# Performance work log

Hardware: AMD Instinct MI355X
Metric: run time of the kernel (lower is better)

The kernel has to match this reference:

```python
import jax, jax.numpy as jnp
import numpy as np

WEIGHT = 1.0
EPS = 1e-10


def _high_mask(h, w):
    # Boolean mask: True = high-frequency region (outside center rectangle after fftshift)
    mask = np.ones((h, w), dtype=np.float32)
    ch, cw = h // 2, w // 2
    mask[ch - h // 8: ch + h // 8, cw - w // 8: cw + w // 8] = 0.0
    return jnp.asarray(mask)


def _high_freq_psd(img):
    # img: (B, 3, H, W) in [-1, 1] -> per-image mean log10 PSD over high-freq region, shape (B,)
    gray = 0.299 * img[:, 0] + 0.587 * img[:, 1] + 0.114 * img[:, 2]  # (B, H, W)
    gray = (gray + 1.0) / 2.0
    fft = jnp.fft.fft2(gray)                       # batched complex FFT over last two dims
    fft = jnp.fft.fftshift(fft, axes=(-2, -1))
    psd_log = jnp.log10(jnp.abs(fft) ** 2 + EPS)   # (B, H, W)
    h, w = gray.shape[-2:]
    mask = _high_mask(h, w)
    return jnp.sum(psd_log * mask, axis=(-2, -1)) / jnp.sum(mask)


def setup_inputs() -> dict:
    key = jax.random.key(0)
    k1, k2 = jax.random.split(key)
    B, C, H, W = 32, 3, 512, 512
    generated = jax.random.normal(k1, (B, C, H, W), dtype=jnp.float32)
    target = jax.random.normal(k2, (B, C, H, W), dtype=jnp.float32)
    return {"generated": generated, "target": target}


def reference(generated, target):
    psd_gen = _high_freq_psd(generated)      # (B,)
    psd_target = _high_freq_psd(target)      # (B,)
    loss = jnp.mean(jnp.abs(psd_gen - psd_target))  # F.l1_loss
    return WEIGHT * loss
```

## Files before the change

### kernel.cpp

```cpp
#include <hip/hip_runtime.h>
#include <hip/hip_bf16.h>
#include <hip/hip_fp16.h>
#include <math.h>


__device__ double g_partials[64 * 33 * 4];
__device__ __align__(16) __half2 g_wsfall[256 * 512];

__device__ __forceinline__ float2 cadd(float2 a, float2 b){ return make_float2(a.x+b.x, a.y+b.y); }
__device__ __forceinline__ float2 csub(float2 a, float2 b){ return make_float2(a.x-b.x, a.y-b.y); }
__device__ __forceinline__ float2 cmul(float2 a, float2 b){
  return make_float2(fmaf(a.x, b.x, -(a.y*b.y)), fmaf(a.x, b.y, a.y*b.x));
}
__device__ __forceinline__ float2 mul_mi(float2 a){ return make_float2(a.y, -a.x); }

__device__ __forceinline__ void fft8(float2 v[8]){
  const float S = 0.70710678118654752440f;
  float2 c0=cadd(v[0],v[4]), c1=cadd(v[1],v[5]), c2=cadd(v[2],v[6]), c3=cadd(v[3],v[7]);
  float2 d0=csub(v[0],v[4]);
  float2 t1=csub(v[1],v[5]);
  float2 d1=make_float2(S*(t1.x+t1.y), S*(t1.y-t1.x));
  float2 d2=mul_mi(csub(v[2],v[6]));
  float2 t3=csub(v[3],v[7]);
  float2 d3=make_float2(S*(t3.y-t3.x), -S*(t3.x+t3.y));
  float2 e0=cadd(c0,c2), e1=cadd(c1,c3), f0=csub(c0,c2), f1=mul_mi(csub(c1,c3));
  float2 g0=cadd(d0,d2), g1=cadd(d1,d3), h0=csub(d0,d2), h1=mul_mi(csub(d1,d3));
  v[0]=cadd(e0,e1); v[4]=csub(e0,e1);
  v[2]=cadd(f0,f1); v[6]=csub(f0,f1);
  v[1]=cadd(g0,g1); v[5]=csub(g0,g1);
  v[3]=cadd(h0,h1); v[7]=csub(h0,h1);
}

__device__ __forceinline__ void twiddle8(float2 v[8], float ang){
  float sn, cs;
  __sincosf(ang, &sn, &cs);
  float2 w = make_float2(cs, sn);
  float2 wp = w;
  v[1] = cmul(v[1], wp);
  #pragma unroll
  for (int m = 2; m < 8; ++m){ wp = cmul(wp, w); v[m] = cmul(v[m], wp); }
}

__device__ __forceinline__ int padi(int i){ return i + (i >> 3); }

__device__ __forceinline__ void lds_fence(){
  asm volatile("s_waitcnt lgkmcnt(0)" ::: "memory");
  __builtin_amdgcn_sched_barrier(0);
}

__device__ __forceinline__ void fft512(float2 v[8], float* re, float* im, int t){
  const float TW = -6.28318530717958647692f;
  fft8(v);
  twiddle8(v, TW * (float)t * (1.0f/512.0f));
  lds_fence();
  #pragma unroll
  for (int m = 0; m < 8; ++m){ int a = padi(m*64 + t); re[a] = v[m].x; im[a] = v[m].y; }
  lds_fence();
  const int q = t >> 3, n = t & 7;
  #pragma unroll
  for (int j = 0; j < 8; ++j){ int a = padi(q*64 + n + 8*j); v[j].x = re[a]; v[j].y = im[a]; }
  fft8(v);
  twiddle8(v, TW * (float)n * (1.0f/64.0f));
  lds_fence();
  #pragma unroll
  for (int m = 0; m < 8; ++m){ int a = padi(q*64 + m*8 + n); re[a] = v[m].x; im[a] = v[m].y; }
  lds_fence();
  #pragma unroll
  for (int j = 0; j < 8; ++j){ int a = padi(q*64 + n*8 + j); v[j].x = re[a]; v[j].y = im[a]; }
  fft8(v);
}

#define GRAY1(r,g,b) ((fmaf(0.299f,(r), fmaf(0.587f,(g), 0.114f*(b))) + 1.0f)*0.5f)

__device__ __forceinline__ void dma_pair(const float* base, float* st, int t){
  #pragma unroll
  for (int ch = 0; ch < 3; ++ch){
    const float* pb = base + ch * 262144 + 4*t;
    float* lb = st + ch*1024;
    #pragma unroll
    for (int seg = 0; seg < 4; ++seg){
      __builtin_amdgcn_global_load_lds(
        (const __attribute__((address_space(1))) void*)(pb + seg*256),
        (__attribute__((address_space(3))) void*)(lb + seg*256),
        16, 0, 0);
    }
  }
}

__global__ __launch_bounds__(128)
void k_rowfft(const float* __restrict__ gen, const float* __restrict__ tgt,
              __half2* ws, int img0){
  __half2* w = ws ? ws : g_wsfall;
  const int wg   = blockIdx.x;
  const int imgl = wg >> 4;
  const int bl   = wg & 15;
  const int img  = img0 + imgl;
  const int wave = threadIdx.x >> 6, t = threadIdx.x & 63;
  const int prB  = bl*16 + wave*8;
  const float* src = (img < 32) ? gen : tgt;
  const float* base0 = src + (size_t)(img & 31) * 786432 + (size_t)prB * 1024;

  __shared__ float stage_all[2][2][3072];
  float* stg0 = stage_all[wave][0];
  float* stg1 = stage_all[wave][1];

  const int off = 8*(t & 7) + (t >> 3);

  dma_pair(base0, stg0, t);
  #pragma unroll
  for (int n = 0; n < 8; ++n){
    float* stc = (n & 1) ? stg1 : stg0;
    float* stn = (n & 1) ? stg0 : stg1;
    lds_fence();
    if (n < 7) dma_pair(base0 + (size_t)(n+1)*1024, stn, t);
    if (n == 0)      { asm volatile("s_waitcnt vmcnt(12)" ::: "memory"); }
    else if (n < 7)  { asm volatile("s_waitcnt vmcnt(20)" ::: "memory"); }
    else             { asm volatile("s_waitcnt vmcnt(8)"  ::: "memory"); }
    __builtin_amdgcn_sched_barrier(0);

    float2 v[8];
    #pragma unroll
    for (int j = 0; j < 8; ++j){
      const int x = t + 64*j;
      v[j] = make_float2(GRAY1(stc[x],     stc[1024+x], stc[2048+x]),
                         GRAY1(stc[512+x], stc[1536+x], stc[2560+x]));
    }
    fft512(v, stc, stc + 1024, t);

    __half2* dst = w + ((size_t)imgl * 256 + (prB + n)) * 512;
    #pragma unroll
    for (int j = 0; j < 8; ++j) dst[64*j + off] = __floats2half2_rn(v[j].x, v[j].y);
  }
}

__global__ __launch_bounds__(256)
void k_colfft(const __half2* __restrict__ ws, int img0){
  const __half2* w = ws ? ws : (const __half2*)g_wsfall;
  const int wg   = blockIdx.x;
  const int imgl = wg / 33;
  const int blk  = wg - imgl * 33;
  const int img  = img0 + imgl;
  const int kx0  = blk * 8;
  const int tid  = threadIdx.x;
  const int wave = tid >> 6, t = tid & 63;
  const int ncols = (blk == 32) ? 1 : 8;

  __shared__ float2 own[8][260], mir[8][260];
  __shared__ float re_all[4][576], im_all[4][576];
  float* re = re_all[wave];
  float* im = im_all[wave];

  const __half2* zb = w + (size_t)imgl * 131072;
  #pragma unroll
  for (int it = 0; it < 8; ++it){
    const int idx = it*256 + tid;
    const int p = idx >> 3, e = idx & 7;
    own[e][p] = __half22float2(zb[p*512 + kx0 + e]);
    mir[e][p] = __half22float2(zb[p*512 + ((512 - (kx0 + e)) & 511)]);
  }
  __syncthreads();

  double acc = 0.0;
  for (int ci = 0; ci < 2; ++ci){
    const int e = wave*2 + ci;
    if (e < ncols){
      const int kx = kx0 + e;
      const bool sub_own = (kx <= 63);
      const bool sub_mir = (kx >= 1) & (kx <= 64);
      const float base = (kx == 0 || kx == 256) ? 1.0f : 2.0f;

      float2 v[8];
      const int u = t >> 1;
      const bool odd = (t & 1);
      #pragma unroll
      for (int j = 0; j < 8; ++j){
        const int p = u + 32*j;
        float2 A = own[e][p];
        float2 B = mir[e][p]; B.y = -B.y;
        float2 Fe = make_float2((A.x + B.x)*0.5f, (A.y + B.y)*0.5f);
        float2 Fo = mul_mi(make_float2((A.x - B.x)*0.5f, (A.y - B.y)*0.5f));
        v[j] = odd ? Fo : Fe;
      }
      fft512(v, re, im, t);

      #pragma unroll
      for (int j = 0; j < 8; ++j){
        const bool inS  = (j == 0) | (j == 7);
        const bool inSp = (j == 0) | ((j == 1) & (t == 0)) | ((j == 7) & (t != 0));
        float wgt = base;
        if (sub_own & inS)  wgt -= 1.0f;
        if (sub_mir & inSp) wgt -= 1.0f;
        float m2 = fmaf(v[j].x, v[j].x, fmaf(v[j].y, v[j].y, 1e-10f));
        acc += (double)wgt * (double)log10f(m2);
      }
    }
  }
  #pragma unroll
  for (int off = 32; off; off >>= 1) acc += __shfl_down(acc, off);
  if (t == 0) g_partials[((size_t)img * 33 + blk) * 4 + wave] = acc;
}

__global__ __launch_bounds__(256)
void k_finish(float* __restrict__ out){
  const int tid = threadIdx.x;
  const int img = tid >> 2, part = tid & 3;
  const double* p = g_partials + (size_t)img * 132 + part;
  double s = 0.0;
  for (int k = 0; k < 33; ++k) s += p[4*k];
  __shared__ double sm[256];
  sm[tid] = s;
  __syncthreads();
  if ((tid & 3) == 0){
    double tot = sm[tid] + sm[tid+1] + sm[tid+2] + sm[tid+3];
    sm[tid] = tot * (1.0 / 245760.0);
  }
  __syncthreads();
  if (tid < 64){
    double dv = (tid < 32) ? fabs(sm[tid*4] - sm[(tid+32)*4]) : 0.0;
    #pragma unroll
    for (int off = 32; off; off >>= 1) dv += __shfl_down(dv, off);
    if (tid == 0) out[0] = (float)(dv * (1.0 / 32.0));
  }
}

extern "C" void kernel_launch(void* const* d_in, const int* in_sizes, int n_in,
                              void* d_out, int out_size, void* d_ws, size_t ws_size,
                              hipStream_t stream){
  (void)in_sizes; (void)n_in; (void)out_size;
  const float* gen = (const float*)d_in[0];
  const float* tgt = (const float*)d_in[1];
  float* out = (float*)d_out;

  const size_t per_img = (size_t)256 * 512 * sizeof(__half2);
  int chunk = (int)(ws_size / per_img);
  __half2* wsp = (__half2*)d_ws;
  if (chunk < 1){ chunk = 1; wsp = nullptr; }
  if (chunk > 64) chunk = 64;

  for (int i0 = 0; i0 < 64; i0 += chunk){
    const int n = (64 - i0 < chunk) ? (64 - i0) : chunk;
    k_rowfft<<<dim3(n * 16), dim3(128), 0, stream>>>(gen, tgt, wsp, i0);
    k_colfft<<<dim3(n * 33), dim3(256), 0, stream>>>(wsp, i0);
  }
  k_finish<<<dim3(1), dim3(256), 0, stream>>>(out);
}
```

Baseline: 72.44 us.

## Use static full-size workspace and process 16 columns per column-FFT block

Replaces the chunked workspace loop with a static device buffer sized for all 64 images, so only one row-FFT and one column-FFT launch are issued. The column kernel now handles 16 columns per block (17 blocks per image, four columns per wave) and keeps the staged columns in LDS as half2 rather than float2. This cuts launch overhead and per-block fixed cost, though each block does more serial work and there are fewer blocks in flight.

```diff
diff --git a/kernel.cpp b/kernel.cpp
--- a/kernel.cpp
+++ b/kernel.cpp
@@ -4,8 +4,8 @@
 #include <math.h>
 
 
-__device__ double g_partials[64 * 33 * 4];
-__device__ __align__(16) __half2 g_wsfall[256 * 512];
+__device__ double g_partials[64 * 17 * 4];
+__device__ __align__(16) __half2 g_ws[(size_t)64 * 256 * 512];
 
 __device__ __forceinline__ float2 cadd(float2 a, float2 b){ return make_float2(a.x+b.x, a.y+b.y); }
 __device__ __forceinline__ float2 csub(float2 a, float2 b){ return make_float2(a.x-b.x, a.y-b.y); }
@@ -88,13 +88,10 @@
 }
 
 __global__ __launch_bounds__(128)
-void k_rowfft(const float* __restrict__ gen, const float* __restrict__ tgt,
-              __half2* ws, int img0){
-  __half2* w = ws ? ws : g_wsfall;
+void k_rowfft(const float* __restrict__ gen, const float* __restrict__ tgt){
   const int wg   = blockIdx.x;
-  const int imgl = wg >> 4;
+  const int img  = wg >> 4;
   const int bl   = wg & 15;
-  const int img  = img0 + imgl;
   const int wave = threadIdx.x >> 6, t = threadIdx.x & 63;
   const int prB  = bl*16 + wave*8;
   const float* src = (img < 32) ? gen : tgt;
@@ -127,42 +124,40 @@
     }
     fft512(v, stc, stc + 1024, t);
 
-    __half2* dst = w + ((size_t)imgl * 256 + (prB + n)) * 512;
+    __half2* dst = g_ws + ((size_t)img * 256 + (prB + n)) * 512;
     #pragma unroll
     for (int j = 0; j < 8; ++j) dst[64*j + off] = __floats2half2_rn(v[j].x, v[j].y);
   }
 }
 
 __global__ __launch_bounds__(256)
-void k_colfft(const __half2* __restrict__ ws, int img0){
-  const __half2* w = ws ? ws : (const __half2*)g_wsfall;
+void k_colfft(){
   const int wg   = blockIdx.x;
-  const int imgl = wg / 33;
-  const int blk  = wg - imgl * 33;
-  const int img  = img0 + imgl;
-  const int kx0  = blk * 8;
+  const int img  = wg / 17;
+  const int blk  = wg - img * 17;
+  const int kx0  = blk * 16;
   const int tid  = threadIdx.x;
   const int wave = tid >> 6, t = tid & 63;
-  const int ncols = (blk == 32) ? 1 : 8;
-
-  __shared__ float2 own[8][260], mir[8][260];
+  const int ncols = (blk == 16) ? 1 : 16;
+
+  __shared__ __half2 own[16 * 258], mir[16 * 258];
   __shared__ float re_all[4][576], im_all[4][576];
   float* re = re_all[wave];
   float* im = im_all[wave];
 
-  const __half2* zb = w + (size_t)imgl * 131072;
-  #pragma unroll
-  for (int it = 0; it < 8; ++it){
+  const __half2* zb = g_ws + (size_t)img * 131072;
+  #pragma unroll
+  for (int it = 0; it < 16; ++it){
     const int idx = it*256 + tid;
-    const int p = idx >> 3, e = idx & 7;
-    own[e][p] = __half22float2(zb[p*512 + kx0 + e]);
-    mir[e][p] = __half22float2(zb[p*512 + ((512 - (kx0 + e)) & 511)]);
+    const int p = idx >> 4, e = idx & 15;
+    own[e*258 + p] = zb[p*512 + kx0 + e];
+    mir[e*258 + p] = zb[p*512 + ((512 - (kx0 + e)) & 511)];
   }
   __syncthreads();
 
   double acc = 0.0;
-  for (int ci = 0; ci < 2; ++ci){
-    const int e = wave*2 + ci;
+  for (int ci = 0; ci < 4; ++ci){
+    const int e = wave*4 + ci;
     if (e < ncols){
       const int kx = kx0 + e;
       const bool sub_own = (kx <= 63);
@@ -175,8 +170,8 @@
       #pragma unroll
       for (int j = 0; j < 8; ++j){
         const int p = u + 32*j;
-        float2 A = own[e][p];
-        float2 B = mir[e][p]; B.y = -B.y;
+        float2 A = __half22float2(own[e*258 + p]);
+        float2 B = __half22float2(mir[e*258 + p]); B.y = -B.y;
         float2 Fe = make_float2((A.x + B.x)*0.5f, (A.y + B.y)*0.5f);
         float2 Fo = mul_mi(make_float2((A.x - B.x)*0.5f, (A.y - B.y)*0.5f));
         v[j] = odd ? Fo : Fe;
@@ -197,16 +192,16 @@
   }
   #pragma unroll
   for (int off = 32; off; off >>= 1) acc += __shfl_down(acc, off);
-  if (t == 0) g_partials[((size_t)img * 33 + blk) * 4 + wave] = acc;
+  if (t == 0) g_partials[((size_t)img * 17 + blk) * 4 + wave] = acc;
 }
 
 __global__ __launch_bounds__(256)
 void k_finish(float* __restrict__ out){
   const int tid = threadIdx.x;
   const int img = tid >> 2, part = tid & 3;
-  const double* p = g_partials + (size_t)img * 132 + part;
+  const double* p = g_partials + (size_t)img * 68 + part;
   double s = 0.0;
-  for (int k = 0; k < 33; ++k) s += p[4*k];
+  for (int k = 0; k < 17; ++k) s += p[4*k];
   __shared__ double sm[256];
   sm[tid] = s;
   __syncthreads();
@@ -226,21 +221,12 @@
 extern "C" void kernel_launch(void* const* d_in, const int* in_sizes, int n_in,
                               void* d_out, int out_size, void* d_ws, size_t ws_size,
                               hipStream_t stream){
-  (void)in_sizes; (void)n_in; (void)out_size;
+  (void)in_sizes; (void)n_in; (void)out_size; (void)d_ws; (void)ws_size;
   const float* gen = (const float*)d_in[0];
   const float* tgt = (const float*)d_in[1];
   float* out = (float*)d_out;
 
-  const size_t per_img = (size_t)256 * 512 * sizeof(__half2);
-  int chunk = (int)(ws_size / per_img);
-  __half2* wsp = (__half2*)d_ws;
-  if (chunk < 1){ chunk = 1; wsp = nullptr; }
-  if (chunk > 64) chunk = 64;
-
-  for (int i0 = 0; i0 < 64; i0 += chunk){
-    const int n = (64 - i0 < chunk) ? (64 - i0) : chunk;
-    k_rowfft<<<dim3(n * 16), dim3(128), 0, stream>>>(gen, tgt, wsp, i0);
-    k_colfft<<<dim3(n * 33), dim3(256), 0, stream>>>(wsp, i0);
-  }
+  k_rowfft<<<dim3(64 * 16), dim3(128), 0, stream>>>(gen, tgt);
+  k_colfft<<<dim3(64 * 17), dim3(256), 0, stream>>>();
   k_finish<<<dim3(1), dim3(256), 0, stream>>>(out);
 }
```

Result: faster. 70.64 us, median of 2 (-2.5%).
